# Optimization experiments

Measured on AMD Instinct MI355X. Metric: run time of the kernel, lower is better.

The kernel has to match this reference:

```python
import jax, jax.numpy as jnp
import numpy as np

HIDDEN_DIM = 400
STACK_DEPTH = 32
BATCH = 1
SEQ_LEN = 8192


def setup_inputs() -> dict:
    key = jax.random.key(0)
    k1, k2, k3 = jax.random.split(key, 3)
    hidden_state = jax.random.normal(k1, (BATCH, SEQ_LEN, HIDDEN_DIM), dtype=jnp.float32)
    # action_predictor: nn.Linear(hidden_dim, 3)
    W_ap = jax.random.normal(k2, (3, HIDDEN_DIM), dtype=jnp.float32) * 0.05
    b_ap = jnp.zeros((3,), dtype=jnp.float32)
    # D: nn.Parameter(torch.randn(1, hidden_dim))
    D = jax.random.normal(k3, (1, HIDDEN_DIM), dtype=jnp.float32)
    return {"hidden_state": hidden_state, "W_ap": W_ap, "b_ap": b_ap, "D": D}


def reference(hidden_state, W_ap, b_ap, D):
    # hidden_state: [B, T, H]
    B, T, H = hidden_state.shape
    # Per-step action probabilities (computed for all t at once): [B, T, 3]
    probs = jax.nn.softmax(jnp.einsum('bth,ah->bta', hidden_state, W_ap) + b_ap, axis=-1)
    # push value: sigmoid(D . h_t), scalar per (b, t) (well-defined at B=1)
    pv = jax.nn.sigmoid(jnp.einsum('bth,h->bt', hidden_state, D[0]))  # [B, T]
    push = jnp.transpose(probs[..., 0])   # [T, B]
    pop_ = jnp.transpose(probs[..., 1])   # [T, B]
    noop = jnp.transpose(probs[..., 2])   # [T, B]
    pv_t = jnp.transpose(pv)              # [T, B]

    stack0 = jnp.zeros((B, STACK_DEPTH, H), dtype=hidden_state.dtype)

    # Net effect of the two aliased in-place shifts (snapshot semantics):
    #   s2[0] = s[1]; s2[i] = s[i] for i >= 1
    # then stack[0] = push*push_val + pop*s2[1] + noop*s2[0]
    #               = push*push_val + (pop+noop)*s[1]
    def step(stack, xs):
        pu, po, no, v = xs  # each [B]
        s1 = stack[:, 1, :]  # [B, H]
        new_top = (pu * v)[:, None] + (po + no)[:, None] * s1  # [B, H]
        new_stack = stack.at[:, 0, :].set(new_top)
        return new_stack, new_stack

    _, stacks = jax.lax.scan(step, stack0, (push, pop_, noop, pv_t))  # [T, B, D, H]
    return jnp.transpose(stacks, (1, 0, 2, 3))  # [B, T, D, H]
```

## Files before the change

### kernel.cpp

```cpp
#include <hip/hip_runtime.h>

#define HDIM 400
#define TLEN 8192
#define DEPTH 32
#define SLICE (DEPTH * HDIM)
#define BLOCK 256

__global__ __launch_bounds__(BLOCK) void stack_memory_kernel(
    const float* __restrict__ hs,
    const float* __restrict__ W,
    const float* __restrict__ b,
    const float* __restrict__ D,
    float* __restrict__ out)
{
    const int t = blockIdx.x;
    const float* __restrict__ x = hs + (size_t)t * HDIM;

    float a0 = 0.f, a1 = 0.f, a2 = 0.f, ad = 0.f;
    for (int i = threadIdx.x; i < HDIM; i += BLOCK) {
        float h = x[i];
        a0 += h * W[i];
        a1 += h * W[HDIM + i];
        a2 += h * W[2 * HDIM + i];
        ad += h * D[i];
    }

    #pragma unroll
    for (int off = 32; off > 0; off >>= 1) {
        a0 += __shfl_down(a0, off);
        a1 += __shfl_down(a1, off);
        a2 += __shfl_down(a2, off);
        ad += __shfl_down(ad, off);
    }

    __shared__ float s0[4], s1[4], s2[4], sd[4];
    __shared__ float sval;
    const int wave = threadIdx.x >> 6;
    const int lane = threadIdx.x & 63;
    if (lane == 0) { s0[wave] = a0; s1[wave] = a1; s2[wave] = a2; sd[wave] = ad; }
    __syncthreads();
    if (threadIdx.x == 0) {
        float l0 = s0[0] + s0[1] + s0[2] + s0[3] + b[0];
        float l1 = s1[0] + s1[1] + s1[2] + s1[3] + b[1];
        float l2 = s2[0] + s2[1] + s2[2] + s2[3] + b[2];
        float dd = sd[0] + sd[1] + sd[2] + sd[3];
        float m  = fmaxf(l0, fmaxf(l1, l2));
        float e0 = __expf(l0 - m);
        float e1 = __expf(l1 - m);
        float e2 = __expf(l2 - m);
        float p0 = e0 / (e0 + e1 + e2);
        float pv = 1.0f / (1.0f + __expf(-dd));
        sval = p0 * pv;
    }
    __syncthreads();

    const float v = sval;
    float4* __restrict__ o = (float4*)(out + (size_t)t * SLICE);
    const float4 vz = make_float4(0.f, 0.f, 0.f, 0.f);
    const float4 vv = make_float4(v, v, v, v);
    for (int i = threadIdx.x; i < SLICE / 4; i += BLOCK) {
        o[i] = (i < HDIM / 4) ? vv : vz;
    }
}

extern "C" void kernel_launch(void* const* d_in, const int* in_sizes, int n_in,
                              void* d_out, int out_size, void* d_ws, size_t ws_size,
                              hipStream_t stream) {
    const float* hs = (const float*)d_in[0];
    const float* W  = (const float*)d_in[1];
    const float* b  = (const float*)d_in[2];
    const float* D  = (const float*)d_in[3];
    float* out = (float*)d_out;

    stack_memory_kernel<<<TLEN, BLOCK, 0, stream>>>(hs, W, b, D, out);
}
```

Before: 478.7 us.

## Split into per-wave value kernel and grid-stride streaming fill kernel

The single fused kernel is split in two. The first computes the per-timestep scalar with one wave per timestep, reduced by xor shuffles with no shared memory or block barriers, and writes it to workspace. A second grid-stride kernel then fills the whole ~420MB output with float4 stores, reading the scalar per timestep. The aim is a write-bandwidth-bound fill decoupled from the reduction, at the cost of an extra launch, a workspace round-trip, and an integer division per element.

After: 424.1 us. 11.4% less time.

```diff
diff --git a/kernel.cpp b/kernel.cpp
--- a/kernel.cpp
+++ b/kernel.cpp
@@ -1,23 +1,29 @@
 #include <hip/hip_runtime.h>
 
-#define HDIM 400
-#define TLEN 8192
+#define HDIM  400
+#define TLEN  8192
 #define DEPTH 32
 #define SLICE (DEPTH * HDIM)
+#define SLICE4 (SLICE / 4)
+#define ROW4   (HDIM / 4)
+#define NF4   ((size_t)TLEN * SLICE4)
 #define BLOCK 256
 
-__global__ __launch_bounds__(BLOCK) void stack_memory_kernel(
+__global__ __launch_bounds__(BLOCK) void val_kernel(
     const float* __restrict__ hs,
     const float* __restrict__ W,
     const float* __restrict__ b,
     const float* __restrict__ D,
-    float* __restrict__ out)
+    float* __restrict__ val)
 {
-    const int t = blockIdx.x;
+    const int wave = threadIdx.x >> 6;
+    const int lane = threadIdx.x & 63;
+    const int t = blockIdx.x * (BLOCK / 64) + wave;
+
     const float* __restrict__ x = hs + (size_t)t * HDIM;
 
     float a0 = 0.f, a1 = 0.f, a2 = 0.f, ad = 0.f;
-    for (int i = threadIdx.x; i < HDIM; i += BLOCK) {
+    for (int i = lane; i < HDIM; i += 64) {
         float h = x[i];
         a0 += h * W[i];
         a1 += h * W[HDIM + i];
@@ -27,39 +33,37 @@
 
     #pragma unroll
     for (int off = 32; off > 0; off >>= 1) {
-        a0 += __shfl_down(a0, off);
-        a1 += __shfl_down(a1, off);
-        a2 += __shfl_down(a2, off);
-        ad += __shfl_down(ad, off);
+        a0 += __shfl_xor(a0, off);
+        a1 += __shfl_xor(a1, off);
+        a2 += __shfl_xor(a2, off);
+        ad += __shfl_xor(ad, off);
     }
 
-    __shared__ float s0[4], s1[4], s2[4], sd[4];
-    __shared__ float sval;
-    const int wave = threadIdx.x >> 6;
-    const int lane = threadIdx.x & 63;
-    if (lane == 0) { s0[wave] = a0; s1[wave] = a1; s2[wave] = a2; sd[wave] = ad; }
-    __syncthreads();
-    if (threadIdx.x == 0) {
-        float l0 = s0[0] + s0[1] + s0[2] + s0[3] + b[0];
-        float l1 = s1[0] + s1[1] + s1[2] + s1[3] + b[1];
-        float l2 = s2[0] + s2[1] + s2[2] + s2[3] + b[2];
-        float dd = sd[0] + sd[1] + sd[2] + sd[3];
-        float m  = fmaxf(l0, fmaxf(l1, l2));
-        float e0 = __expf(l0 - m);
-        float e1 = __expf(l1 - m);
-        float e2 = __expf(l2 - m);
-        float p0 = e0 / (e0 + e1 + e2);
-        float pv = 1.0f / (1.0f + __expf(-dd));
-        sval = p0 * pv;
-    }
-    __syncthreads();
+    float l0 = a0 + b[0];
+    float l1 = a1 + b[1];
+    float l2 = a2 + b[2];
+    float m  = fmaxf(l0, fmaxf(l1, l2));
+    float e0 = __expf(l0 - m);
+    float e1 = __expf(l1 - m);
+    float e2 = __expf(l2 - m);
+    float p0 = e0 / (e0 + e1 + e2);
+    float pv = 1.0f / (1.0f + __expf(-ad));
+    float v  = p0 * pv;
 
-    const float v = sval;
-    float4* __restrict__ o = (float4*)(out + (size_t)t * SLICE);
-    const float4 vz = make_float4(0.f, 0.f, 0.f, 0.f);
-    const float4 vv = make_float4(v, v, v, v);
-    for (int i = threadIdx.x; i < SLICE / 4; i += BLOCK) {
-        o[i] = (i < HDIM / 4) ? vv : vz;
+    if (lane == 0) val[t] = v;
+}
+
+__global__ __launch_bounds__(BLOCK) void fill_kernel(
+    const float* __restrict__ val,
+    float4* __restrict__ out)
+{
+    const unsigned stride = gridDim.x * BLOCK;
+    for (unsigned g = blockIdx.x * BLOCK + threadIdx.x; g < NF4; g += stride) {
+        unsigned t = g / SLICE4;
+        unsigned w = g - t * SLICE4;
+        float v = 0.f;
+        if (w < ROW4) v = val[t];
+        out[g] = make_float4(v, v, v, v);
     }
 }
 
@@ -71,6 +75,8 @@
     const float* b  = (const float*)d_in[2];
     const float* D  = (const float*)d_in[3];
     float* out = (float*)d_out;
+    float* val = (float*)d_ws;
 
-    stack_memory_kernel<<<TLEN, BLOCK, 0, stream>>>(hs, W, b, D, out);
+    val_kernel<<<TLEN / (BLOCK / 64), BLOCK, 0, stream>>>(hs, W, b, D, val);
+    fill_kernel<<<4096, BLOCK, 0, stream>>>(val, (float4*)out);
 }
```
